# Kernel optimization log

Measured on AMD Instinct MI355X. Metric: run time of the kernel, lower is better.

Reference implementation:

```python
import jax, jax.numpy as jnp
import numpy as np
from jax import lax

B, T, C = 4, 2048, 2048
H, S = 32, 64
HEAD_SIZE_DIVISOR = 8.0
LN_EPS = 1e-5


def setup_inputs() -> dict:
    key = jax.random.key(0)
    ks = jax.random.split(key, 12)
    scale = 0.02
    return {
        "hidden": jax.random.normal(ks[0], (B, T, C), jnp.float32),
        "state_kv": jnp.zeros((B, H, S, S), jnp.float32),
        "time_decay": jax.random.normal(ks[1], (H, S), jnp.float32) * 0.5,
        "time_faaaa": jax.random.normal(ks[2], (H, S), jnp.float32) * 0.5,
        "time_mix_key": jax.random.uniform(ks[3], (1, 1, C), jnp.float32),
        "time_mix_value": jax.random.uniform(ks[4], (1, 1, C), jnp.float32),
        "time_mix_receptance": jax.random.uniform(ks[5], (1, 1, C), jnp.float32),
        "time_mix_gate": jax.random.uniform(ks[6], (1, 1, C), jnp.float32),
        "key_w": jax.random.normal(ks[7], (C, C), jnp.float32) * scale,
        "value_w": jax.random.normal(ks[8], (C, C), jnp.float32) * scale,
        "receptance_w": jax.random.normal(ks[9], (C, C), jnp.float32) * scale,
        "gate_w": jax.random.normal(ks[10], (C, C), jnp.float32) * scale,
        "output_w": jax.random.normal(ks[11], (C, C), jnp.float32) * scale,
        "ln_w": jnp.ones((C,), jnp.float32),
        "ln_b": jnp.zeros((C,), jnp.float32),
    }


def _rwkv5_scan(r, k, v, w, u, state0):
    # r,k,v: [B,T,H,S]; w,u: [H,S]; state0: [B,H,S,S]
    w_ = w[None, :, :, None]  # decay broadcast over value dim
    u_ = u[None, :, :, None]  # time_first (bonus) broadcast over value dim

    def step(state, rkv):
        rt, kt, vt = rkv  # each [B,H,S]
        a = kt[:, :, :, None] * vt[:, :, None, :]      # outer product [B,H,S,S]
        o = jnp.einsum("bhs,bhsd->bhd", rt, u_ * a + state)
        state = a + w_ * state
        return state, o

    rt = jnp.moveaxis(r, 1, 0)  # [T,B,H,S]
    kt = jnp.moveaxis(k, 1, 0)
    vt = jnp.moveaxis(v, 1, 0)
    state_f, out = lax.scan(step, state0, (rt, kt, vt))
    return jnp.moveaxis(out, 0, 1), state_f  # [B,T,H,S], [B,H,S,S]


def reference(hidden, state_kv, time_decay, time_faaaa, time_mix_key,
              time_mix_value, time_mix_receptance, time_mix_gate,
              key_w, value_w, receptance_w, gate_w, output_w, ln_w, ln_b):
    B_, T_, C_ = hidden.shape
    H_, S_ = time_faaaa.shape

    # time shift: prepend zero row, drop last (state=None path)
    shifted = jnp.pad(hidden, ((0, 0), (1, 0), (0, 0)))[:, :-1]

    mix = lambda m: hidden * m + shifted * (1.0 - m)
    k = mix(time_mix_key) @ key_w.T
    v = mix(time_mix_value) @ value_w.T
    r = mix(time_mix_receptance) @ receptance_w.T
    gate = jax.nn.silu(mix(time_mix_gate) @ gate_w.T)

    r = r.reshape(B_, T_, H_, S_)
    k = k.reshape(B_, T_, H_, S_)
    v = v.reshape(B_, T_, H_, S_)

    w = jnp.exp(-jnp.exp(time_decay))  # [H,S]
    out, state_f = _rwkv5_scan(r, k, v, w, time_faaaa, state_kv)

    # GroupNorm over H groups of size S, applied per (b,t) row
    x = out.reshape(B_ * T_, H_, S_) / HEAD_SIZE_DIVISOR
    mu = jnp.mean(x, axis=-1, keepdims=True)
    var = jnp.var(x, axis=-1, keepdims=True)
    xn = (x - mu) * lax.rsqrt(var + LN_EPS)
    xn = xn.reshape(B_ * T_, H_ * S_) * ln_w + ln_b

    out = xn.reshape(B_, T_, C_) * gate
    out = out @ output_w.T
    return out, state_f
```

## Files before the change

### kernel.cpp

```cpp
#include <hip/hip_runtime.h>
#include <hip/hip_bf16.h>

typedef unsigned short u16;
typedef __bf16 bf16x8 __attribute__((ext_vector_type(8)));
typedef unsigned short ushort8v __attribute__((ext_vector_type(8)));
typedef float f32x4 __attribute__((ext_vector_type(4)));
typedef float f32x8 __attribute__((ext_vector_type(8)));

#define B_ 4
#define T_ 2048
#define C_ 2048
#define H_ 32
#define S_ 64

__device__ __forceinline__ u16 f2bf(float x) {
  unsigned int u = __float_as_uint(x);
  unsigned int r = (u + 0x7fffu + ((u >> 16) & 1u)) >> 16;
  return (u16)r;
}
__device__ __forceinline__ float bf2f(u16 x) {
  return __uint_as_float(((unsigned int)x) << 16);
}
__device__ __forceinline__ void gload_lds16(const void* g, void* l) {
  __builtin_amdgcn_global_load_lds(
      (const __attribute__((address_space(1))) void*)g,
      (__attribute__((address_space(3))) void*)l, 16, 0, 0);
}

#define VM10 asm volatile("s_waitcnt vmcnt(10)" ::: "memory")
#define VM8 asm volatile("s_waitcnt vmcnt(8)" ::: "memory")
#define VM4 asm volatile("s_waitcnt vmcnt(4)" ::: "memory")
#define VM0 asm volatile("s_waitcnt vmcnt(0)" ::: "memory")
#define BARR __builtin_amdgcn_s_barrier()
#define SCB __builtin_amdgcn_sched_barrier(0)

__global__ __launch_bounds__(256) void mix_cast_kernel(
    const float* __restrict__ hidden, const float* __restrict__ mixp,
    u16* __restrict__ out) {
  int idx = blockIdx.x * 256 + threadIdx.x;
  int c4 = idx & 511;
  int bt = idx >> 9;
  int t = bt & (T_ - 1);
  float4 h = reinterpret_cast<const float4*>(hidden)[idx];
  float4 m = reinterpret_cast<const float4*>(mixp)[c4];
  float4 sh = make_float4(0.f, 0.f, 0.f, 0.f);
  if (t != 0) sh = reinterpret_cast<const float4*>(hidden)[idx - 512];
  ushort4 o;
  o.x = f2bf(h.x * m.x + sh.x * (1.f - m.x));
  o.y = f2bf(h.y * m.y + sh.y * (1.f - m.y));
  o.z = f2bf(h.z * m.z + sh.z * (1.f - m.z));
  o.w = f2bf(h.w * m.w + sh.w * (1.f - m.w));
  reinterpret_cast<ushort4*>(out)[idx] = o;
}

__global__ __launch_bounds__(256) void mix4_cast_kernel(
    const float* __restrict__ hidden,
    const float* __restrict__ mK, const float* __restrict__ mV,
    const float* __restrict__ mR, const float* __restrict__ mG,
    u16* __restrict__ oK, u16* __restrict__ oV,
    u16* __restrict__ oR, u16* __restrict__ oG) {
  int idx = blockIdx.x * 256 + threadIdx.x;
  int c4 = idx & 511;
  int bt = idx >> 9;
  int t = bt & (T_ - 1);
  float4 h = reinterpret_cast<const float4*>(hidden)[idx];
  float4 sh = make_float4(0.f, 0.f, 0.f, 0.f);
  if (t != 0) sh = reinterpret_cast<const float4*>(hidden)[idx - 512];
  float4 m;
  ushort4 o;
#define DOMIX(MP, OP)                                          \
  m = reinterpret_cast<const float4*>(MP)[c4];                 \
  o.x = f2bf(h.x * m.x + sh.x * (1.f - m.x));                  \
  o.y = f2bf(h.y * m.y + sh.y * (1.f - m.y));                  \
  o.z = f2bf(h.z * m.z + sh.z * (1.f - m.z));                  \
  o.w = f2bf(h.w * m.w + sh.w * (1.f - m.w));                  \
  reinterpret_cast<ushort4*>(OP)[idx] = o;
  DOMIX(mK, oK)
  DOMIX(mV, oV)
  DOMIX(mR, oR)
  DOMIX(mG, oG)
#undef DOMIX
}

__global__ __launch_bounds__(256) void conv_bf16_kernel(
    const float* __restrict__ in, u16* __restrict__ out, int n4) {
  int i = blockIdx.x * 256 + threadIdx.x;
  if (i >= n4) return;
  float4 v = reinterpret_cast<const float4*>(in)[i];
  ushort4 o;
  o.x = f2bf(v.x); o.y = f2bf(v.y); o.z = f2bf(v.z); o.w = f2bf(v.w);
  reinterpret_cast<ushort4*>(out)[i] = o;
}

__global__ __launch_bounds__(256) void conv4_bf16_kernel(
    const float* __restrict__ w0, const float* __restrict__ w1,
    const float* __restrict__ w2, const float* __restrict__ w3,
    u16* __restrict__ o0, u16* __restrict__ o1,
    u16* __restrict__ o2, u16* __restrict__ o3) {
  int wsel = blockIdx.x >> 12;
  int i = (blockIdx.x & 4095) * 256 + threadIdx.x;
  const float* in = (wsel == 0) ? w0 : (wsel == 1) ? w1 : (wsel == 2) ? w2 : w3;
  u16* out = (wsel == 0) ? o0 : (wsel == 1) ? o1 : (wsel == 2) ? o2 : o3;
  float4 v = reinterpret_cast<const float4*>(in)[i];
  ushort4 o;
  o.x = f2bf(v.x); o.y = f2bf(v.y); o.z = f2bf(v.z); o.w = f2bf(v.w);
  reinterpret_cast<ushort4*>(out)[i] = o;
}

template <typename OT>
__global__ __launch_bounds__(512, 2) void gemm_bt256(
    const u16* __restrict__ A, const u16* __restrict__ Bm,
    OT* __restrict__ C, int M, int N, int K) {
  __shared__ u16 Asl[4][8192];
  __shared__ u16 Bsl[4][8192];
  const int tid = threadIdx.x, lane = tid & 63, w = tid >> 6;
  const int wr = w >> 2, wc = w & 3;
  const int a15 = lane & 15, g4 = lane >> 4;
  const int nbn = N >> 8;
  const int nwg = gridDim.x, bid = blockIdx.x, cpx = nwg >> 3;
  const int swz = (bid & 7) * cpx + (bid >> 3);
  const int bm = swz / nbn, bn = swz % nbn;
  const int Ar0 = bm * 256, Br0 = bn * 256;

  const int rowoff = w * 32 + (lane >> 2);
  const int colswz = ((lane & 3) ^ ((lane >> 3) & 3)) * 8;
  const u16* Agl = A + (size_t)(Ar0 + rowoff) * K + colswz;
  const u16* Bgl = Bm + (size_t)(Br0 + rowoff) * K + colswz;
  const int lb = w * 1024;

  const int rdc = (((lane >> 4) ^ ((lane >> 1) & 3))) * 8;
  const int arow = wr * 128 + a15;
  const int brow = wc * 64 + a15;

  f32x4 acc[8][4];
#pragma unroll
  for (int m = 0; m < 8; m++)
#pragma unroll
    for (int n = 0; n < 4; n++) acc[m][n] = (f32x4){0.f, 0.f, 0.f, 0.f};

  auto STA = [&](int ktile, int kk, int slot) {
    const u16* g = Agl + ktile * 64 + kk * 32;
    gload_lds16(g, &Asl[slot][lb]);
    gload_lds16(g + (size_t)16 * K, &Asl[slot][lb + 512]);
  };
  auto STB = [&](int ktile, int kk, int slot) {
    const u16* g = Bgl + ktile * 64 + kk * 32;
    gload_lds16(g, &Bsl[slot][lb]);
    gload_lds16(g + (size_t)16 * K, &Bsl[slot][lb + 512]);
  };
  auto PHK = [&](int P, int kk) {
    const u16* As_ = Asl[P * 2 + kk];
    const u16* Bs_ = Bsl[P * 2 + kk];
    bf16x8 af[8], bv[4];
#pragma unroll
    for (int mf = 0; mf < 8; mf++)
      af[mf] = __builtin_bit_cast(
          bf16x8, *reinterpret_cast<const ushort8v*>(&As_[(arow + mf * 16) * 32 + rdc]));
#pragma unroll
    for (int nf = 0; nf < 4; nf++)
      bv[nf] = __builtin_bit_cast(
          bf16x8, *reinterpret_cast<const ushort8v*>(&Bs_[(brow + nf * 16) * 32 + rdc]));
    __builtin_amdgcn_s_setprio(1);
#pragma unroll
    for (int mf = 0; mf < 8; mf++)
#pragma unroll
      for (int nf = 0; nf < 4; nf++)
        acc[mf][nf] =
            __builtin_amdgcn_mfma_f32_16x16x32_bf16(af[mf], bv[nf], acc[mf][nf], 0, 0, 0);
    __builtin_amdgcn_s_setprio(0);
  };

  const int NT = K >> 6;
  STA(0, 0, 0); STB(0, 0, 0);
  STA(0, 1, 1); STB(0, 1, 1);
  STA(1, 0, 2); STB(1, 0, 2);

  for (int T = 0; T + 2 < NT; ++T) {
    int P = T & 1, Q = P ^ 1;
    STA(T + 1, 1, Q * 2 + 1); STB(T + 1, 1, Q * 2 + 1);
    VM10; BARR; SCB; PHK(P, 0); BARR;
    STA(T + 2, 0, P * 2 + 0); STB(T + 2, 0, P * 2 + 0);
    VM10; BARR; SCB; PHK(P, 1); BARR;
  }
  {
    int T = NT - 2, P = T & 1, Q = P ^ 1;
    STA(T + 1, 1, Q * 2 + 1); STB(T + 1, 1, Q * 2 + 1);
    VM10; BARR; SCB; PHK(P, 0); BARR;
    VM8; BARR; SCB; PHK(P, 1); BARR;
  }
  {
    int P = (NT - 1) & 1;
    VM4; BARR; SCB; PHK(P, 0); BARR;
    VM0; BARR; SCB; PHK(P, 1); BARR;
  }

  if constexpr (sizeof(OT) == 2) {
    u16* ep = (w < 4) ? Asl[w] : Bsl[w - 4];
#pragma unroll
    for (int mfg = 0; mfg < 8; mfg++)
#pragma unroll
      for (int q = 0; q < 4; q++)
#pragma unroll
        for (int nf = 0; nf < 4; nf++)
          ep[(mfg * 16 + g4 * 4 + q) * 64 + nf * 16 + a15] = f2bf(acc[mfg][nf][q]);
    OT* cbase = C + (size_t)(Ar0 + wr * 128) * N + Br0 + wc * 64;
#pragma unroll
    for (int i = 0; i < 16; i++) {
      int id = lane + 64 * i;
      int row = id >> 3, k16 = id & 7;
      ushort8v v8 = *reinterpret_cast<const ushort8v*>(&ep[row * 64 + k16 * 8]);
      *reinterpret_cast<ushort8v*>(cbase + (size_t)row * N + k16 * 8) = v8;
    }
  } else {
    int crow0 = Ar0 + wr * 128 + g4 * 4;
    int ccol0 = Br0 + wc * 64 + a15;
#pragma unroll
    for (int mfg = 0; mfg < 8; mfg++) {
#pragma unroll
      for (int q = 0; q < 4; q++) {
        OT* cp = C + (size_t)(crow0 + mfg * 16 + q) * N + ccol0;
#pragma unroll
        for (int nf = 0; nf < 4; nf++) cp[nf * 16] = (OT)acc[mfg][nf][q];
      }
    }
  }
}

template <int CHL>
__global__ __launch_bounds__(64) void scan_phase1_mfma(
    const u16* __restrict__ Kb, const u16* __restrict__ Vb,
    const float* __restrict__ td, float* __restrict__ chunks) {
  constexpr int NCH = T_ / CHL;
  constexpr int LDW = CHL + 8;
  __shared__ u16 Ash[64 * LDW];
  __shared__ u16 Vsh[64 * LDW];
  int lane = threadIdx.x & 63;
  int gw = blockIdx.x;
  int c = gw & (NCH - 1), bh = gw / NCH;
  int h = bh & 31, b = bh >> 5;

  size_t base = ((size_t)b * T_ + (size_t)c * CHL) * C_ + h * 64 + lane;
  const u16* Kp = Kb + base;
  const u16* Vp = Vb + base;

  {
    float w = __expf(-__expf(td[h * 64 + lane]));
    u16* Arow = &Ash[lane * LDW];
    float p = 1.f;
#pragma unroll
    for (int i4 = CHL - 4; i4 >= 0; i4 -= 4) {
      float a3 = bf2f(Kp[(size_t)(i4 + 3) * C_]) * p; p *= w;
      float a2 = bf2f(Kp[(size_t)(i4 + 2) * C_]) * p; p *= w;
      float a1 = bf2f(Kp[(size_t)(i4 + 1) * C_]) * p; p *= w;
      float a0 = bf2f(Kp[(size_t)(i4 + 0) * C_]) * p; p *= w;
      ushort4 pk;
      pk.x = f2bf(a0); pk.y = f2bf(a1); pk.z = f2bf(a2); pk.w = f2bf(a3);
      *reinterpret_cast<ushort4*>(&Arow[i4]) = pk;
    }
  }
  {
    u16* Vrow = &Vsh[lane * LDW];
#pragma unroll
    for (int i4 = 0; i4 < CHL; i4 += 4) {
      ushort4 pk;
      pk.x = Vp[(size_t)(i4 + 0) * C_];
      pk.y = Vp[(size_t)(i4 + 1) * C_];
      pk.z = Vp[(size_t)(i4 + 2) * C_];
      pk.w = Vp[(size_t)(i4 + 3) * C_];
      *reinterpret_cast<ushort4*>(&Vrow[i4]) = pk;
    }
  }

  f32x4 acc[4][4];
#pragma unroll
  for (int m = 0; m < 4; m++)
#pragma unroll
    for (int n = 0; n < 4; n++) acc[m][n] = (f32x4){0.f, 0.f, 0.f, 0.f};

#pragma unroll
  for (int kb = 0; kb < CHL / 32; kb++) {
    int ko = kb * 32 + (lane >> 4) * 8;
    bf16x8 Af[4], Bf[4];
#pragma unroll
    for (int m = 0; m < 4; m++) {
      ushort8v t8 = *reinterpret_cast<const ushort8v*>(&Ash[(m * 16 + (lane & 15)) * LDW + ko]);
      Af[m] = __builtin_bit_cast(bf16x8, t8);
    }
#pragma unroll
    for (int n = 0; n < 4; n++) {
      ushort8v t8 = *reinterpret_cast<const ushort8v*>(&Vsh[(n * 16 + (lane & 15)) * LDW + ko]);
      Bf[n] = __builtin_bit_cast(bf16x8, t8);
    }
#pragma unroll
    for (int m = 0; m < 4; m++)
#pragma unroll
      for (int n = 0; n < 4; n++)
        acc[m][n] = __builtin_amdgcn_mfma_f32_16x16x32_bf16(Af[m], Bf[n], acc[m][n], 0, 0, 0);
  }

  float* outp = chunks + (((size_t)c * B_ + b) * H_ + h) * 4096;
  int r0 = (lane >> 4) * 4, c0 = lane & 15;
#pragma unroll
  for (int m = 0; m < 4; m++)
#pragma unroll
    for (int n = 0; n < 4; n++)
#pragma unroll
      for (int q = 0; q < 4; q++)
        outp[(size_t)(m * 16 + r0 + q) * 64 + n * 16 + c0] = acc[m][n][q];
}

template <int NCH, int CHL>
__global__ __launch_bounds__(256) void scan_phase1(
    const u16* __restrict__ Kb, const u16* __restrict__ Vb,
    const float* __restrict__ td, float* __restrict__ chunks) {
  int lane = threadIdx.x & 63;
  int gw = (blockIdx.x * 256 + threadIdx.x) >> 6;
  int c = gw & (NCH - 1), bh = gw / NCH;
  int h = bh & 31, b = bh >> 5;
  const float* tdh = td + h * 64;
  float wreg[64];
#pragma unroll
  for (int s = 0; s < 64; s++) wreg[s] = __expf(-__expf(tdh[s]));
  float st[64];
#pragma unroll
  for (int s = 0; s < 64; s++) st[s] = 0.f;
  size_t base = ((size_t)b * T_ + (size_t)c * CHL) * C_ + h * 64 + lane;
  const u16* Kp = Kb + base;
  const u16* Vp = Vb + base;
  for (int t = 0; t < CHL; t++) {
    float kcur = bf2f(Kp[(size_t)t * C_]), vcur = bf2f(Vp[(size_t)t * C_]);
#pragma unroll
    for (int s = 0; s < 64; s++) {
      float ks = __shfl(kcur, s);
      st[s] = fmaf(wreg[s], st[s], ks * vcur);
    }
  }
  float* outp = chunks + (((size_t)c * B_ + b) * H_ + h) * 4096 + lane;
#pragma unroll
  for (int s = 0; s < 64; s++) outp[s * 64] = st[s];
}

template <int NCH, int CHL>
__global__ __launch_bounds__(256) void scan_phase2(
    const float* __restrict__ st0, const float* __restrict__ td,
    float* __restrict__ chunks, float* __restrict__ state_out) {
  int idx = blockIdx.x * 256 + threadIdx.x;
  int h = (idx >> 12) & 31;
  int s = (idx >> 6) & 63;
  float wL = __expf(-(float)CHL * __expf(td[h * 64 + s]));
  float st = st0[idx];
#pragma unroll
  for (int cc = 0; cc < NCH; cc++) {
    size_t off = (size_t)cc * 524288 + idx;
    float sc = chunks[off];
    chunks[off] = st;
    st = fmaf(wL, st, sc);
  }
  state_out[idx] = st;
}

__global__ __launch_bounds__(256) void scan_phase3_mfma(
    const u16* __restrict__ Rb, const u16* __restrict__ Kb,
    const u16* __restrict__ Vb, const float* __restrict__ td,
    const float* __restrict__ tf, const float* __restrict__ chunks,
    const u16* __restrict__ Gb, const float* __restrict__ lnw,
    const float* __restrict__ lnb, u16* __restrict__ Y) {
  __shared__ __align__(16) u16 smem[4][5248];
  int lane = threadIdx.x & 63, wib = threadIdx.x >> 6;
  int gw = blockIdx.x * 4 + wib;
  int c = gw & 31, bh = gw >> 5;
  int h = bh & 31, b = bh >> 5;
  int a = lane & 15, g = lane >> 4;
  int h0 = h * 64;

  u16* Kt = smem[wib];
  u16* Vt = Kt + 1024;
  u16* StT = Vt + 1024;
  u16* AT = StT + 2560;

  f32x8 sA[2], sB[2], sC[2];
#pragma unroll
  for (int kk = 0; kk < 2; kk++) {
#pragma unroll
    for (int e = 0; e < 8; e++) {
      int s = kk * 32 + g * 8 + e;
      float ew = __expf(td[h0 + s]);
      sA[kk][e] = __expf(-(float)a * ew);
      sB[kk][e] = __expf(-((float)a - 8.f) * ew);
      sC[kk][e] = __expf(-(7.f - (float)a) * ew);
    }
  }
  f32x4 sE[4];
  f32x4 ewD;
#pragma unroll
  for (int ms = 0; ms < 4; ms++) {
    ewD[ms] = __expf(td[h0 + ms * 16 + a]);
#pragma unroll
    for (int q = 0; q < 4; q++)
      sE[ms][q] = __expf(-16.f * __expf(td[h0 + ms * 16 + g * 4 + q]));
  }

  f32x4 St[4][4];
  const float* cpc = chunks + (((size_t)c * B_ + b) * H_ + h) * 4096;
#pragma unroll
  for (int ms = 0; ms < 4; ms++)
#pragma unroll
    for (int nd = 0; nd < 4; nd++)
#pragma unroll
      for (int q = 0; q < 4; q++)
        St[ms][nd][q] = cpc[(size_t)(ms * 16 + g * 4 + q) * 64 + nd * 16 + a];

#pragma unroll
  for (int z = 0; z < 6; z++) {
    int idx = z * 64 + lane;
    int row = idx / 24, col = 16 + idx % 24;
    AT[row * 40 + col] = 0;
  }

  size_t tbase = ((size_t)b * T_ + (size_t)c * 64) * C_ + h0;

  for (int sb = 0; sb < 4; sb++) {
    size_t rb0 = tbase + (size_t)(sb * 16) * C_;

    ushort8v r8[2], k8[2];
#pragma unroll
    for (int kk = 0; kk < 2; kk++) {
      r8[kk] = *reinterpret_cast<const ushort8v*>(Rb + rb0 + (size_t)a * C_ + kk * 32 + g * 8);
      k8[kk] = *reinterpret_cast<const ushort8v*>(Kb + rb0 + (size_t)a * C_ + kk * 32 + g * 8);
    }
    {
      int srow = lane >> 3;
      int scol = (lane & 7) * 8;
      *reinterpret_cast<ushort8v*>(&Kt[srow * 64 + scol]) =
          *reinterpret_cast<const ushort8v*>(Kb + rb0 + (size_t)srow * C_ + scol);
      *reinterpret_cast<ushort8v*>(&Kt[(srow + 8) * 64 + scol]) =
          *reinterpret_cast<const ushort8v*>(Kb + rb0 + (size_t)(srow + 8) * C_ + scol);
      *reinterpret_cast<ushort8v*>(&Vt[srow * 64 + scol]) =
          *reinterpret_cast<const ushort8v*>(Vb + rb0 + (size_t)srow * C_ + scol);
      *reinterpret_cast<ushort8v*>(&Vt[(srow + 8) * 64 + scol]) =
          *reinterpret_cast<const ushort8v*>(Vb + rb0 + (size_t)(srow + 8) * C_ + scol);
    }

    f32x4 O[4];
#pragma unroll
    for (int nd = 0; nd < 4; nd++) O[nd] = (f32x4){0.f, 0.f, 0.f, 0.f};

#pragma unroll
    for (int kk = 0; kk < 2; kk++) {
#pragma unroll
      for (int msl = 0; msl < 2; msl++) {
        int ms = kk * 2 + msl;
#pragma unroll
        for (int nd = 0; nd < 4; nd++) {
          ushort4 pk;
          pk.x = f2bf(St[ms][nd][0]); pk.y = f2bf(St[ms][nd][1]);
          pk.z = f2bf(St[ms][nd][2]); pk.w = f2bf(St[ms][nd][3]);
          *reinterpret_cast<ushort4*>(&StT[(a + nd * 16) * 40 + msl * 16 + g * 4]) = pk;
        }
      }
      ushort8v rt;
#pragma unroll
      for (int e = 0; e < 8; e++) rt[e] = f2bf(bf2f(r8[kk][e]) * sA[kk][e]);
      bf16x8 rtf = __builtin_bit_cast(bf16x8, rt);
#pragma unroll
      for (int nd = 0; nd < 4; nd++) {
        ushort8v sfr = *reinterpret_cast<const ushort8v*>(&StT[(a + nd * 16) * 40 + g * 8]);
        O[nd] = __builtin_amdgcn_mfma_f32_16x16x32_bf16(
            rtf, __builtin_bit_cast(bf16x8, sfr), O[nd], 0, 0, 0);
      }
    }

    float p = 0.f;
    {
      uintptr_t ta = (uintptr_t)(tf + h0);
      asm volatile("" : "+v"(ta));
      const float* tfp = (const float*)ta;
#pragma unroll
      for (int kk = 0; kk < 2; kk++) {
        float4 t0 = *reinterpret_cast<const float4*>(tfp + kk * 32 + g * 8);
        float4 t1 = *reinterpret_cast<const float4*>(tfp + kk * 32 + g * 8 + 4);
        float tv[8] = {t0.x, t0.y, t0.z, t0.w, t1.x, t1.y, t1.z, t1.w};
#pragma unroll
        for (int e = 0; e < 8; e++)
          p = fmaf(bf2f(r8[kk][e]) * tv[e], bf2f(k8[kk][e]), p);
      }
    }
    p += __shfl_xor(p, 16);
    p += __shfl_xor(p, 32);

    f32x4 Am = (f32x4){0.f, 0.f, 0.f, 0.f};
#pragma unroll
    for (int kk = 0; kk < 2; kk++) {
      ushort8v kh, rh;
#pragma unroll
      for (int e = 0; e < 8; e++) {
        kh[e] = f2bf(bf2f(k8[kk][e]) * sC[kk][e]);
        rh[e] = f2bf(bf2f(r8[kk][e]) * sB[kk][e]);
      }
      Am = __builtin_amdgcn_mfma_f32_16x16x32_bf16(
          __builtin_bit_cast(bf16x8, kh), __builtin_bit_cast(bf16x8, rh), Am, 0, 0, 0);
    }
    {
      ushort4 aw;
#pragma unroll
      for (int q = 0; q < 4; q++) {
        int jr = g * 4 + q;
        float v = (jr < a) ? Am[q] : ((jr == a) ? p : 0.f);
        ((u16*)&aw)[q] = f2bf(v);
      }
      *reinterpret_cast<ushort4*>(&AT[a * 40 + g * 4]) = aw;
    }
    bf16x8 afrag;
    {
      ushort8v t8 = *reinterpret_cast<const ushort8v*>(&AT[a * 40 + g * 8]);
      afrag = __builtin_bit_cast(bf16x8, t8);
    }

    bf16x8 vfrag[4];
#pragma unroll
    for (int nd = 0; nd < 4; nd++) {
      ushort8v t8;
      if (g < 2) {
#pragma unroll
        for (int e = 0; e < 8; e++) t8[e] = Vt[(g * 8 + e) * 64 + a + nd * 16];
      } else {
#pragma unroll
        for (int e = 0; e < 8; e++) t8[e] = 0;
      }
      vfrag[nd] = __builtin_bit_cast(bf16x8, t8);
    }

#pragma unroll
    for (int nd = 0; nd < 4; nd++)
      O[nd] = __builtin_amdgcn_mfma_f32_16x16x32_bf16(afrag, vfrag[nd], O[nd], 0, 0, 0);

#pragma unroll
    for (int ms = 0; ms < 4; ms++)
#pragma unroll
      for (int nd = 0; nd < 4; nd++)
#pragma unroll
        for (int q = 0; q < 4; q++) St[ms][nd][q] *= sE[ms][q];

#pragma unroll
    for (int ms = 0; ms < 4; ms++) {
      ushort8v kt8;
      if (g < 2) {
#pragma unroll
        for (int e = 0; e < 8; e++) {
          int j = g * 8 + e;
          float f = bf2f(Kt[j * 64 + ms * 16 + a]) * __expf(-(15.f - (float)j) * ewD[ms]);
          kt8[e] = f2bf(f);
        }
      } else {
#pragma unroll
        for (int e = 0; e < 8; e++) kt8[e] = 0;
      }
      bf16x8 kf = __builtin_bit_cast(bf16x8, kt8);
#pragma unroll
      for (int nd = 0; nd < 4; nd++)
        St[ms][nd] = __builtin_amdgcn_mfma_f32_16x16x32_bf16(kf, vfrag[nd], St[ms][nd], 0, 0, 0);
    }

#pragma unroll
    for (int nd = 0; nd < 4; nd++)
#pragma unroll
      for (int q = 0; q < 4; q++) O[nd][q] *= 0.125f;
    {
      uintptr_t la = (uintptr_t)(lnw + h0);
      uintptr_t lba = (uintptr_t)(lnb + h0);
      asm volatile("" : "+v"(la), "+v"(lba));
      const float* lwp = (const float*)la;
      const float* lbp = (const float*)lba;
#pragma unroll
      for (int q = 0; q < 4; q++) {
        float ssum = O[0][q] + O[1][q] + O[2][q] + O[3][q];
        ssum += __shfl_xor(ssum, 1); ssum += __shfl_xor(ssum, 2);
        ssum += __shfl_xor(ssum, 4); ssum += __shfl_xor(ssum, 8);
        float mean = ssum * (1.f / 64.f);
        float vv = 0.f;
#pragma unroll
        for (int nd = 0; nd < 4; nd++) {
          float d = O[nd][q] - mean;
          vv = fmaf(d, d, vv);
        }
        vv += __shfl_xor(vv, 1); vv += __shfl_xor(vv, 2);
        vv += __shfl_xor(vv, 4); vv += __shfl_xor(vv, 8);
        float rs = rsqrtf(vv * (1.f / 64.f) + 1e-5f);
        size_t rowoff = rb0 + (size_t)(g * 4 + q) * C_;
#pragma unroll
        for (int nd = 0; nd < 4; nd++) {
          float xn = (O[nd][q] - mean) * rs;
          float gv = bf2f(Gb[rowoff + nd * 16 + a]);
          float sg = gv / (1.f + __expf(-gv));
          Y[rowoff + nd * 16 + a] = f2bf((xn * lwp[nd * 16 + a] + lbp[nd * 16 + a]) * sg);
        }
      }
    }
  }
}

template <int NCH, int CHL>
__global__ __launch_bounds__(256) void scan_phase3(
    const u16* __restrict__ Rb, const u16* __restrict__ Kb,
    const u16* __restrict__ Vb, const float* __restrict__ td,
    const float* __restrict__ tf, const float* __restrict__ chunks,
    const u16* __restrict__ Gb, const float* __restrict__ lnw,
    const float* __restrict__ lnb, u16* __restrict__ Y) {
  int lane = threadIdx.x & 63;
  int gw = (blockIdx.x * 256 + threadIdx.x) >> 6;
  int c = gw & (NCH - 1), bh = gw / NCH;
  int h = bh & 31, b = bh >> 5;
  const float* tdh = td + h * 64;
  float wreg[64];
#pragma unroll
  for (int s = 0; s < 64; s++) wreg[s] = __expf(-__expf(tdh[s]));
  float u_own = tf[h * 64 + lane];
  float lw = lnw[h * 64 + lane];
  float lb = lnb[h * 64 + lane];
  float st[64];
  const float* cp = chunks + (((size_t)c * B_ + b) * H_ + h) * 4096 + lane;
#pragma unroll
  for (int s = 0; s < 64; s++) st[s] = cp[s * 64];
  size_t base = ((size_t)b * T_ + (size_t)c * CHL) * C_ + h * 64 + lane;
  const u16* Rp = Rb + base;
  const u16* Kp = Kb + base;
  const u16* Vp = Vb + base;
  const u16* Gp = Gb + base;
  u16* Yp = Y + base;
  for (int t = 0; t < CHL; t++) {
    float rcur = bf2f(Rp[(size_t)t * C_]);
    float kcur = bf2f(Kp[(size_t)t * C_]);
    float vcur = bf2f(Vp[(size_t)t * C_]);
    float p = rcur * u_own * kcur;
#pragma unroll
    for (int off = 32; off >= 1; off >>= 1) p += __shfl_xor(p, off);
    float acc = 0.f;
#pragma unroll
    for (int s = 0; s < 64; s++) {
      float rs = __shfl(rcur, s);
      float ks = __shfl(kcur, s);
      acc = fmaf(rs, st[s], acc);
      st[s] = fmaf(wreg[s], st[s], ks * vcur);
    }
    float o = fmaf(p, vcur, acc);
    float x = o * 0.125f;
    float sum = x;
#pragma unroll
    for (int off = 32; off >= 1; off >>= 1) sum += __shfl_xor(sum, off);
    float mean = sum * (1.f / 64.f);
    float d = x - mean;
    float v2 = d * d;
#pragma unroll
    for (int off = 32; off >= 1; off >>= 1) v2 += __shfl_xor(v2, off);
    float var = v2 * (1.f / 64.f);
    float xn = d * rsqrtf(var + 1e-5f);
    float gg = bf2f(Gp[(size_t)t * C_]);
    float sg = gg / (1.f + __expf(-gg));
    Yp[(size_t)t * C_] = f2bf((xn * lw + lb) * sg);
  }
}

extern "C" void kernel_launch(void* const* d_in, const int* in_sizes, int n_in,
                              void* d_out, int out_size, void* d_ws, size_t ws_size,
                              hipStream_t stream) {
  const float* hidden = (const float*)d_in[0];
  const float* state0 = (const float*)d_in[1];
  const float* td = (const float*)d_in[2];
  const float* tf = (const float*)d_in[3];
  const float* mk = (const float*)d_in[4];
  const float* mv = (const float*)d_in[5];
  const float* mr = (const float*)d_in[6];
  const float* mg = (const float*)d_in[7];
  const float* kw = (const float*)d_in[8];
  const float* vw = (const float*)d_in[9];
  const float* rw = (const float*)d_in[10];
  const float* gw = (const float*)d_in[11];
  const float* ow = (const float*)d_in[12];
  const float* lnw = (const float*)d_in[13];
  const float* lnb = (const float*)d_in[14];

  float* out = (float*)d_out;
  float* state_f = out + (size_t)B_ * T_ * C_;

  const size_t MBe = (size_t)B_ * T_ * C_;
  const size_t chunks32 = (size_t)32 * B_ * H_ * S_ * S_ * 4;

  size_t bigNeed = 4 * MBe * 2 + (size_t)C_ * C_ * 2 + 4 * MBe * 2 + chunks32;
  bool useBig = (ws_size >= bigNeed);

  dim3 blk(256);
  int mixGrid = (B_ * T_ * C_ / 4) / 256;
  int convN4 = C_ * C_ / 4;
  int convGrid = convN4 / 256;
  int gemmGrid = (B_ * T_ / 256) * (C_ / 256);
  dim3 gblk(512);

  if (useBig) {
    char* ws = (char*)d_ws;
    u16* mixR = (u16*)ws;  ws += MBe * 2;
    u16* mixK = (u16*)ws;  ws += MBe * 2;
    u16* mixV = (u16*)ws;  ws += MBe * 2;
    u16* mixG = (u16*)ws;  ws += MBe * 2;
    u16* wb = (u16*)ws;    ws += (size_t)C_ * C_ * 2;
    u16* rb = (u16*)ws;    ws += MBe * 2;
    u16* kb = (u16*)ws;    ws += MBe * 2;
    u16* vb = (u16*)ws;    ws += MBe * 2;
    u16* gb = (u16*)ws;    ws += MBe * 2;
    float* chunks = (float*)ws;
    u16* wbK = (u16*)chunks;
    u16* wbV = wbK + (size_t)C_ * C_;
    u16* wbG = wbV + (size_t)C_ * C_;

    mix4_cast_kernel<<<mixGrid, blk, 0, stream>>>(hidden, mk, mv, mr, mg,
                                                  mixK, mixV, mixR, mixG);
    conv4_bf16_kernel<<<4 * convGrid, blk, 0, stream>>>(rw, kw, vw, gw,
                                                        wb, wbK, wbV, wbG);
    gemm_bt256<u16><<<gemmGrid, gblk, 0, stream>>>(mixR, wb, rb, B_ * T_, C_, C_);
    gemm_bt256<u16><<<gemmGrid, gblk, 0, stream>>>(mixK, wbK, kb, B_ * T_, C_, C_);
    gemm_bt256<u16><<<gemmGrid, gblk, 0, stream>>>(mixV, wbV, vb, B_ * T_, C_, C_);
    gemm_bt256<u16><<<gemmGrid, gblk, 0, stream>>>(mixG, wbG, gb, B_ * T_, C_, C_);

    scan_phase1_mfma<64><<<B_ * H_ * 32, dim3(64), 0, stream>>>(kb, vb, td, chunks);
    scan_phase2<32, 64><<<2048, blk, 0, stream>>>(state0, td, chunks, state_f);
    scan_phase3_mfma<<<(B_ * H_ * 32) / 4, blk, 0, stream>>>(rb, kb, vb, td, tf, chunks, gb, lnw, lnb, mixR);

    conv_bf16_kernel<<<convGrid, blk, 0, stream>>>(ow, wb, convN4);
    gemm_bt256<float><<<gemmGrid, gblk, 0, stream>>>(mixR, wb, out, B_ * T_, C_, C_);
    return;
  }

  char* ws = (char*)d_ws;
  u16* mixA = (u16*)ws;    ws += MBe * 2;
  u16* wb = (u16*)ws;      ws += (size_t)C_ * C_ * 2;
  u16* rb = (u16*)ws;      ws += MBe * 2;
  u16* kb = (u16*)ws;      ws += MBe * 2;
  u16* vb = (u16*)ws;      ws += MBe * 2;
  u16* gb = (u16*)ws;      ws += MBe * 2;
  float* chunks = (float*)ws;
  size_t fixed = (size_t)(ws - (char*)d_ws);
  bool use32 = (ws_size >= fixed + chunks32);

  mix_cast_kernel<<<mixGrid, blk, 0, stream>>>(hidden, mr, mixA);
  conv_bf16_kernel<<<convGrid, blk, 0, stream>>>(rw, wb, convN4);
  gemm_bt256<u16><<<gemmGrid, gblk, 0, stream>>>(mixA, wb, rb, B_ * T_, C_, C_);
  mix_cast_kernel<<<mixGrid, blk, 0, stream>>>(hidden, mk, mixA);
  conv_bf16_kernel<<<convGrid, blk, 0, stream>>>(kw, wb, convN4);
  gemm_bt256<u16><<<gemmGrid, gblk, 0, stream>>>(mixA, wb, kb, B_ * T_, C_, C_);
  mix_cast_kernel<<<mixGrid, blk, 0, stream>>>(hidden, mv, mixA);
  conv_bf16_kernel<<<convGrid, blk, 0, stream>>>(vw, wb, convN4);
  gemm_bt256<u16><<<gemmGrid, gblk, 0, stream>>>(mixA, wb, vb, B_ * T_, C_, C_);
  mix_cast_kernel<<<mixGrid, blk, 0, stream>>>(hidden, mg, mixA);
  conv_bf16_kernel<<<convGrid, blk, 0, stream>>>(gw, wb, convN4);
  gemm_bt256<u16><<<gemmGrid, gblk, 0, stream>>>(mixA, wb, gb, B_ * T_, C_, C_);

  if (use32) {
    scan_phase1_mfma<64><<<B_ * H_ * 32, dim3(64), 0, stream>>>(kb, vb, td, chunks);
    scan_phase2<32, 64><<<2048, blk, 0, stream>>>(state0, td, chunks, state_f);
    scan_phase3_mfma<<<(B_ * H_ * 32) / 4, blk, 0, stream>>>(rb, kb, vb, td, tf, chunks, gb, lnw, lnb, mixA);
  } else {
    scan_phase1<16, 128><<<(B_ * H_ * 16) / 4, blk, 0, stream>>>(kb, vb, td, chunks);
    scan_phase2<16, 128><<<2048, blk, 0, stream>>>(state0, td, chunks, state_f);
    scan_phase3<16, 128><<<(B_ * H_ * 16) / 4, blk, 0, stream>>>(rb, kb, vb, td, tf, chunks, gb, lnw, lnb, mixA);
  }

  conv_bf16_kernel<<<convGrid, blk, 0, stream>>>(ow, wb, convN4);
  gemm_bt256<float><<<gemmGrid, gblk, 0, stream>>>(mixA, wb, out, B_ * T_, C_, C_);
}
```

Measured before the change: 696.6 us.

## Shrink GEMM LDS pipeline from four-slot to two-slot double buffering

Replaces the four-slot, three-stage-ahead LDS prefetch schedule in the bf16 GEMM with a simple two-slot double buffer that prefetches one 32-wide k-step ahead. The bf16 epilogue is reworked to stage output through the smaller LDS buffers in two halves. This halves shared memory per block, which may help occupancy or reduce LDS pressure, but it shortens how far global loads run ahead of the MFMA work, so load latency may be less hidden.

```diff
diff --git a/kernel.cpp b/kernel.cpp
--- a/kernel.cpp
+++ b/kernel.cpp
@@ -27,8 +27,6 @@
       (__attribute__((address_space(3))) void*)l, 16, 0, 0);
 }
 
-#define VM10 asm volatile("s_waitcnt vmcnt(10)" ::: "memory")
-#define VM8 asm volatile("s_waitcnt vmcnt(8)" ::: "memory")
 #define VM4 asm volatile("s_waitcnt vmcnt(4)" ::: "memory")
 #define VM0 asm volatile("s_waitcnt vmcnt(0)" ::: "memory")
 #define BARR __builtin_amdgcn_s_barrier()
@@ -111,8 +109,8 @@
 __global__ __launch_bounds__(512, 2) void gemm_bt256(
     const u16* __restrict__ A, const u16* __restrict__ Bm,
     OT* __restrict__ C, int M, int N, int K) {
-  __shared__ u16 Asl[4][8192];
-  __shared__ u16 Bsl[4][8192];
+  __shared__ u16 Asl[2][8192];
+  __shared__ u16 Bsl[2][8192];
   const int tid = threadIdx.x, lane = tid & 63, w = tid >> 6;
   const int wr = w >> 2, wc = w & 3;
   const int a15 = lane & 15, g4 = lane >> 4;
@@ -138,19 +136,17 @@
 #pragma unroll
     for (int n = 0; n < 4; n++) acc[m][n] = (f32x4){0.f, 0.f, 0.f, 0.f};
 
-  auto STA = [&](int ktile, int kk, int slot) {
-    const u16* g = Agl + ktile * 64 + kk * 32;
-    gload_lds16(g, &Asl[slot][lb]);
-    gload_lds16(g + (size_t)16 * K, &Asl[slot][lb + 512]);
+  auto STAGE = [&](int step, int slot) {
+    const u16* ga = Agl + step * 32;
+    gload_lds16(ga, &Asl[slot][lb]);
+    gload_lds16(ga + (size_t)16 * K, &Asl[slot][lb + 512]);
+    const u16* gb = Bgl + step * 32;
+    gload_lds16(gb, &Bsl[slot][lb]);
+    gload_lds16(gb + (size_t)16 * K, &Bsl[slot][lb + 512]);
   };
-  auto STB = [&](int ktile, int kk, int slot) {
-    const u16* g = Bgl + ktile * 64 + kk * 32;
-    gload_lds16(g, &Bsl[slot][lb]);
-    gload_lds16(g + (size_t)16 * K, &Bsl[slot][lb + 512]);
-  };
-  auto PHK = [&](int P, int kk) {
-    const u16* As_ = Asl[P * 2 + kk];
-    const u16* Bs_ = Bsl[P * 2 + kk];
+  auto PHK = [&](int slot) {
+    const u16* As_ = Asl[slot];
+    const u16* Bs_ = Bsl[slot];
     bf16x8 af[8], bv[4];
 #pragma unroll
     for (int mf = 0; mf < 8; mf++)
@@ -170,46 +166,43 @@
     __builtin_amdgcn_s_setprio(0);
   };
 
-  const int NT = K >> 6;
-  STA(0, 0, 0); STB(0, 0, 0);
-  STA(0, 1, 1); STB(0, 1, 1);
-  STA(1, 0, 2); STB(1, 0, 2);
-
-  for (int T = 0; T + 2 < NT; ++T) {
-    int P = T & 1, Q = P ^ 1;
-    STA(T + 1, 1, Q * 2 + 1); STB(T + 1, 1, Q * 2 + 1);
-    VM10; BARR; SCB; PHK(P, 0); BARR;
-    STA(T + 2, 0, P * 2 + 0); STB(T + 2, 0, P * 2 + 0);
-    VM10; BARR; SCB; PHK(P, 1); BARR;
-  }
-  {
-    int T = NT - 2, P = T & 1, Q = P ^ 1;
-    STA(T + 1, 1, Q * 2 + 1); STB(T + 1, 1, Q * 2 + 1);
-    VM10; BARR; SCB; PHK(P, 0); BARR;
-    VM8; BARR; SCB; PHK(P, 1); BARR;
-  }
-  {
-    int P = (NT - 1) & 1;
-    VM4; BARR; SCB; PHK(P, 0); BARR;
-    VM0; BARR; SCB; PHK(P, 1); BARR;
+  const int NT2 = K >> 5;
+  STAGE(0, 0);
+  for (int s = 0; s < NT2; ++s) {
+    int sl = s & 1;
+    if (s + 1 < NT2) {
+      STAGE(s + 1, sl ^ 1);
+      VM4;
+    } else {
+      VM0;
+    }
+    BARR; SCB;
+    PHK(sl);
+    BARR;
   }
 
   if constexpr (sizeof(OT) == 2) {
-    u16* ep = (w < 4) ? Asl[w] : Bsl[w - 4];
-#pragma unroll
-    for (int mfg = 0; mfg < 8; mfg++)
-#pragma unroll
-      for (int q = 0; q < 4; q++)
-#pragma unroll
-        for (int nf = 0; nf < 4; nf++)
-          ep[(mfg * 16 + g4 * 4 + q) * 64 + nf * 16 + a15] = f2bf(acc[mfg][nf][q]);
-    OT* cbase = C + (size_t)(Ar0 + wr * 128) * N + Br0 + wc * 64;
-#pragma unroll
-    for (int i = 0; i < 16; i++) {
-      int id = lane + 64 * i;
-      int row = id >> 3, k16 = id & 7;
-      ushort8v v8 = *reinterpret_cast<const ushort8v*>(&ep[row * 64 + k16 * 8]);
-      *reinterpret_cast<ushort8v*>(cbase + (size_t)row * N + k16 * 8) = v8;
+    u16* ep = (w < 4) ? &Asl[w >> 1][(w & 1) * 4096]
+                      : &Bsl[(w - 4) >> 1][((w - 4) & 1) * 4096];
+#pragma unroll
+    for (int half = 0; half < 2; half++) {
+#pragma unroll
+      for (int mm = 0; mm < 4; mm++) {
+        int mfg = half * 4 + mm;
+#pragma unroll
+        for (int q = 0; q < 4; q++)
+#pragma unroll
+          for (int nf = 0; nf < 4; nf++)
+            ep[(mm * 16 + g4 * 4 + q) * 64 + nf * 16 + a15] = f2bf(acc[mfg][nf][q]);
+      }
+      OT* cbase = C + (size_t)(Ar0 + wr * 128 + half * 64) * N + Br0 + wc * 64;
+#pragma unroll
+      for (int i = 0; i < 8; i++) {
+        int id = lane + 64 * i;
+        int row = id >> 3, k16 = id & 7;
+        ushort8v v8 = *reinterpret_cast<const ushort8v*>(&ep[row * 64 + k16 * 8]);
+        *reinterpret_cast<ushort8v*>(cbase + (size_t)row * N + k16 * 8) = v8;
+      }
     }
   } else {
     int crow0 = Ar0 + wr * 128 + g4 * 4;
```

New measurement: 705.6 us. About the same (+1.3%).

## Double-buffer MFMA operand fragments to overlap LDS reads with matrix math

Applied to the files above, without the earlier changes.

Splits the per-phase step into a fragment load and an MFMA step, using two register sets so the next half-tile's LDS reads are issued before the current half-tile's MFMAs run. This is meant to hide LDS read latency inside the GEMM main loop. It needs an extra set of operand registers (12 more bf16x8 values per thread), which may lower occupancy, and it changes the waitcnt and barrier pattern at the tail of the loop.

```diff
diff --git a/kernel.cpp b/kernel.cpp
--- a/kernel.cpp
+++ b/kernel.cpp
@@ -29,8 +29,8 @@
 
 #define VM10 asm volatile("s_waitcnt vmcnt(10)" ::: "memory")
 #define VM8 asm volatile("s_waitcnt vmcnt(8)" ::: "memory")
-#define VM4 asm volatile("s_waitcnt vmcnt(4)" ::: "memory")
 #define VM0 asm volatile("s_waitcnt vmcnt(0)" ::: "memory")
+#define LGKM0 asm volatile("s_waitcnt lgkmcnt(0)" ::: "memory")
 #define BARR __builtin_amdgcn_s_barrier()
 #define SCB __builtin_amdgcn_sched_barrier(0)
 
@@ -148,10 +148,9 @@
     gload_lds16(g, &Bsl[slot][lb]);
     gload_lds16(g + (size_t)16 * K, &Bsl[slot][lb + 512]);
   };
-  auto PHK = [&](int P, int kk) {
+  auto LOADF = [&](int P, int kk, bf16x8 (&af)[8], bf16x8 (&bv)[4]) {
     const u16* As_ = Asl[P * 2 + kk];
     const u16* Bs_ = Bsl[P * 2 + kk];
-    bf16x8 af[8], bv[4];
 #pragma unroll
     for (int mf = 0; mf < 8; mf++)
       af[mf] = __builtin_bit_cast(
@@ -160,6 +159,8 @@
     for (int nf = 0; nf < 4; nf++)
       bv[nf] = __builtin_bit_cast(
           bf16x8, *reinterpret_cast<const ushort8v*>(&Bs_[(brow + nf * 16) * 32 + rdc]));
+  };
+  auto MM = [&](bf16x8 (&af)[8], bf16x8 (&bv)[4]) {
     __builtin_amdgcn_s_setprio(1);
 #pragma unroll
     for (int mf = 0; mf < 8; mf++)
@@ -170,28 +171,50 @@
     __builtin_amdgcn_s_setprio(0);
   };
 
+  bf16x8 f0A[8], f1A[8];
+  bf16x8 f0B[4], f1B[4];
+
   const int NT = K >> 6;
   STA(0, 0, 0); STB(0, 0, 0);
   STA(0, 1, 1); STB(0, 1, 1);
   STA(1, 0, 2); STB(1, 0, 2);
+  VM8;
+  BARR;
+  LOADF(0, 0, f0A, f0B);
 
   for (int T = 0; T + 2 < NT; ++T) {
     int P = T & 1, Q = P ^ 1;
     STA(T + 1, 1, Q * 2 + 1); STB(T + 1, 1, Q * 2 + 1);
-    VM10; BARR; SCB; PHK(P, 0); BARR;
+    VM10; BARR; SCB;
+    LOADF(P, 1, f1A, f1B);
+    MM(f0A, f0B);
+    BARR;
     STA(T + 2, 0, P * 2 + 0); STB(T + 2, 0, P * 2 + 0);
-    VM10; BARR; SCB; PHK(P, 1); BARR;
+    VM10; BARR; SCB;
+    LOADF(Q, 0, f0A, f0B);
+    MM(f1A, f1B);
+    BARR;
   }
   {
     int T = NT - 2, P = T & 1, Q = P ^ 1;
     STA(T + 1, 1, Q * 2 + 1); STB(T + 1, 1, Q * 2 + 1);
-    VM10; BARR; SCB; PHK(P, 0); BARR;
-    VM8; BARR; SCB; PHK(P, 1); BARR;
+    VM10; BARR; SCB;
+    LOADF(P, 1, f1A, f1B);
+    MM(f0A, f0B);
+    BARR;
+    VM8; BARR; SCB;
+    LOADF(Q, 0, f0A, f0B);
+    MM(f1A, f1B);
+    BARR;
   }
   {
     int P = (NT - 1) & 1;
-    VM4; BARR; SCB; PHK(P, 0); BARR;
-    VM0; BARR; SCB; PHK(P, 1); BARR;
+    VM0; BARR; SCB;
+    LOADF(P, 1, f1A, f1B);
+    MM(f0A, f0B);
+    LGKM0;
+    BARR;
+    MM(f1A, f1B);
   }
 
   if constexpr (sizeof(OT) == 2) {
```

Result: no change. 690.1 us (-0.9%).
